# Performance work log

Measured on AMD Instinct MI355X. Metric: run time of the kernel, lower is better.

The kernel has to match this reference:

```python
import jax, jax.numpy as jnp
import numpy as np
import math

N, D, DV, B = 8192, 128, 128, 64
PHI_EPS = 1e-4
NORM_EPS = 1e-8


def _make_omega(dimv=128, dimqk=128, seed=0):
    # Faithful to FavorAttention._omega: QR of uniform blocks, rows renormalized
    # by norms of uniform rows, then transposed -> shape (dimqk, dimv).
    rng = np.random.default_rng(seed)
    nblocks = dimv // dimqk
    blocks = []
    for _ in range(nblocks):
        q, _ = np.linalg.qr(rng.random((dimqk, dimqk)))
        blocks.append(q.T)
    missing = dimv - nblocks * dimqk
    if missing > 0:
        q, _ = np.linalg.qr(rng.random((dimqk, dimqk)))
        blocks.append(q.T[:missing])
    norm = np.linalg.norm(rng.random((dimv, dimqk)), axis=1, keepdims=True)
    return (norm * np.vstack(blocks)).T.astype(np.float32)


def setup_inputs() -> dict:
    key = jax.random.key(0)
    kq, kk, kv, kb = jax.random.split(key, 4)
    Q = jax.random.normal(kq, (N, D), dtype=jnp.float32)
    K = jax.random.normal(kk, (N, D), dtype=jnp.float32)
    V = jax.random.normal(kv, (N, DV), dtype=jnp.float32)
    batch_seg = jnp.sort(jax.random.randint(kb, (N,), 0, B)).astype(jnp.int64)
    omega = jnp.asarray(_make_omega(128, 128))
    return {"Q": Q, "K": K, "V": V, "omega": omega,
            "batch_seg": batch_seg, "num_batch": B}


def _phi(x, omega, is_query, batch_seg, num_batch):
    d = x.shape[-1]
    m = omega.shape[-1]
    U = (x / d ** 0.25) @ omega                              # [n, m]
    h = jnp.sum(x * x, axis=-1, keepdims=True) / (2.0 * d ** 0.5)
    if is_query:
        maximum = jnp.max(U, axis=-1, keepdims=True)         # per-row max
    else:
        # per-segment max of masked U; original masks off-segment entries with 0,
        # so the effective per-segment max is clamped at 0.
        row_max = jnp.max(U, axis=-1)                        # [n]
        seg_max = jax.ops.segment_max(row_max, batch_seg, num_segments=num_batch)
        seg_max = jnp.maximum(seg_max, 0.0)
        maximum = seg_max[batch_seg][:, None]                # [n, 1]
    return (jnp.exp(U - h - maximum) + PHI_EPS) / math.sqrt(m)


def reference(Q, K, V, omega, batch_seg, num_batch):
    # FAVOR+ linear attention with segment-wise (per-molecule) normalization.
    Qp = _phi(Q, omega, True, batch_seg, num_batch)          # [n, m]
    Kp = _phi(K, omega, False, batch_seg, num_batch)         # [n, m]
    # norm_i = Qp_i . sum_{j in seg(i)} Kp_j  + eps
    Ksum = jax.ops.segment_sum(Kp, batch_seg, num_segments=num_batch)  # [B, m]
    norm = jnp.einsum('nm,nm->n', Qp, Ksum[batch_seg]) + NORM_EPS      # [n]
    # S_b = sum_{j in b} Kp_j (outer) V_j ; equals the masked (K Q^T)^T V of the
    # original, without materializing the n x n matrix.
    S = jax.ops.segment_sum(Kp[:, :, None] * V[:, None, :], batch_seg,
                            num_segments=num_batch)          # [B, m, dv]
    out = jnp.einsum('nm,nmd->nd', Qp, S[batch_seg]) / norm[:, None]
    return out
```

## Files before the change

### kernel.cpp

```cpp
#include <hip/hip_runtime.h>
#include <math.h>


#define NROWS 8192
#define DIM   128
#define NSEG  64

#define INV_D4      0.29730177875068026f
#define INV_SQRT_M  0.08838834764831845f
#define PHI_EPS_F   1e-4f
#define NORM_EPS_F  1e-8f

__global__ __launch_bounds__(256, 4) void k_phi(
    const float* __restrict__ Q, const float* __restrict__ K,
    const float* __restrict__ omega, const int* __restrict__ seg,
    float* __restrict__ Qp, float* __restrict__ UK,
    float* __restrict__ hK, int* __restrict__ segmax)
{
    __shared__ float xs[16][DIM];

    const int t = threadIdx.x;
    const int bid = blockIdx.x;
    const bool isQ = bid < 512;
    const int rowbase = (isQ ? bid : bid - 512) * 16;
    const float* X = (isQ ? Q : K) + (size_t)rowbase * DIM;

    {
        const float4* xg = (const float4*)X;
        float4* xd = (float4*)&xs[0][0];
#pragma unroll
        for (int s = 0; s < 2; ++s) {
            float4 v = xg[t + s * 256];
            v.x *= INV_D4; v.y *= INV_D4; v.z *= INV_D4; v.w *= INV_D4;
            xd[t + s * 256] = v;
        }
    }
    __syncthreads();

    const int w = t >> 6, lane = t & 63;
    const int rg = lane >> 5, cl = lane & 31;
    const int rA = w * 4 + rg * 2, rB = rA + 1;

    float hA, hB;
    {
        const float4 a = *(const float4*)&xs[rA][cl * 4];
        const float4 b = *(const float4*)&xs[rB][cl * 4];
        float pa = a.x * a.x + a.y * a.y + a.z * a.z + a.w * a.w;
        float pb = b.x * b.x + b.y * b.y + b.z * b.z + b.w * b.w;
#pragma unroll
        for (int m = 1; m < 32; m <<= 1) {
            pa += __shfl_xor(pa, m, 64);
            pb += __shfl_xor(pb, m, 64);
        }
        hA = 0.5f * pa; hB = 0.5f * pb;
    }

    float4 accA = make_float4(0.f, 0.f, 0.f, 0.f);
    float4 accB = make_float4(0.f, 0.f, 0.f, 0.f);

#pragma unroll 2
    for (int d = 0; d < DIM; d += 4) {
        const float4 o0 = *(const float4*)&omega[(size_t)(d + 0) * DIM + cl * 4];
        const float4 o1 = *(const float4*)&omega[(size_t)(d + 1) * DIM + cl * 4];
        const float4 o2 = *(const float4*)&omega[(size_t)(d + 2) * DIM + cl * 4];
        const float4 o3 = *(const float4*)&omega[(size_t)(d + 3) * DIM + cl * 4];
        const float4 xa = *(const float4*)&xs[rA][d];
        const float4 xb = *(const float4*)&xs[rB][d];
        accA.x = fmaf(xa.x, o0.x, fmaf(xa.y, o1.x, fmaf(xa.z, o2.x, fmaf(xa.w, o3.x, accA.x))));
        accA.y = fmaf(xa.x, o0.y, fmaf(xa.y, o1.y, fmaf(xa.z, o2.y, fmaf(xa.w, o3.y, accA.y))));
        accA.z = fmaf(xa.x, o0.z, fmaf(xa.y, o1.z, fmaf(xa.z, o2.z, fmaf(xa.w, o3.z, accA.z))));
        accA.w = fmaf(xa.x, o0.w, fmaf(xa.y, o1.w, fmaf(xa.z, o2.w, fmaf(xa.w, o3.w, accA.w))));
        accB.x = fmaf(xb.x, o0.x, fmaf(xb.y, o1.x, fmaf(xb.z, o2.x, fmaf(xb.w, o3.x, accB.x))));
        accB.y = fmaf(xb.x, o0.y, fmaf(xb.y, o1.y, fmaf(xb.z, o2.y, fmaf(xb.w, o3.y, accB.y))));
        accB.z = fmaf(xb.x, o0.z, fmaf(xb.y, o1.z, fmaf(xb.z, o2.z, fmaf(xb.w, o3.z, accB.z))));
        accB.w = fmaf(xb.x, o0.w, fmaf(xb.y, o1.w, fmaf(xb.z, o2.w, fmaf(xb.w, o3.w, accB.w))));
    }

    float mA = fmaxf(fmaxf(accA.x, accA.y), fmaxf(accA.z, accA.w));
    float mB = fmaxf(fmaxf(accB.x, accB.y), fmaxf(accB.z, accB.w));
#pragma unroll
    for (int m = 1; m < 32; m <<= 1) {
        mA = fmaxf(mA, __shfl_xor(mA, m, 64));
        mB = fmaxf(mB, __shfl_xor(mB, m, 64));
    }

    const int gA = rowbase + rA, gB = rowbase + rB;
    if (isQ) {
        const float bA = hA + mA, bB = hB + mB;
        float4 eA, eB;
        eA.x = (__expf(accA.x - bA) + PHI_EPS_F) * INV_SQRT_M;
        eA.y = (__expf(accA.y - bA) + PHI_EPS_F) * INV_SQRT_M;
        eA.z = (__expf(accA.z - bA) + PHI_EPS_F) * INV_SQRT_M;
        eA.w = (__expf(accA.w - bA) + PHI_EPS_F) * INV_SQRT_M;
        eB.x = (__expf(accB.x - bB) + PHI_EPS_F) * INV_SQRT_M;
        eB.y = (__expf(accB.y - bB) + PHI_EPS_F) * INV_SQRT_M;
        eB.z = (__expf(accB.z - bB) + PHI_EPS_F) * INV_SQRT_M;
        eB.w = (__expf(accB.w - bB) + PHI_EPS_F) * INV_SQRT_M;
        *(float4*)&Qp[(size_t)gA * DIM + cl * 4] = eA;
        *(float4*)&Qp[(size_t)gB * DIM + cl * 4] = eB;
    } else {
        *(float4*)&UK[(size_t)gA * DIM + cl * 4] = accA;
        *(float4*)&UK[(size_t)gB * DIM + cl * 4] = accB;
        if (cl == 0) {
            hK[gA] = hA; hK[gB] = hB;
            if (mA > 0.f) atomicMax(&segmax[seg[gA]], __float_as_int(mA));
            if (mB > 0.f) atomicMax(&segmax[seg[gB]], __float_as_int(mB));
        }
    }
}

__global__ __launch_bounds__(256, 4) void k_accum(
    const float* __restrict__ UK, const float* __restrict__ hK,
    const float* __restrict__ V, const int* __restrict__ seg,
    const float* __restrict__ segmaxf,
    float* __restrict__ S, float* __restrict__ Ksum)
{
    __shared__ float kp[32][32];
    __shared__ float vv[32][32];

    const int t = threadIdx.x;
    const int sid  = blockIdx.x >> 4;
    const int tile = blockIdx.x & 15;
    const int tm = (tile >> 2) * 32;
    const int tv = (tile & 3) * 32;

    int start, end;
    {
        int a = 0, b = NROWS;
        while (a < b) { int m = (a + b) >> 1; if (seg[m] < sid) a = m + 1; else b = m; }
        start = a; b = NROWS;
        while (a < b) { int m = (a + b) >> 1; if (seg[m] < sid + 1) a = m + 1; else b = m; }
        end = a;
    }

    const float smax = segmaxf[sid];
    const int rs = t >> 3;
    const int cs = (t & 7) * 4;
    const int ty = t >> 4;
    const int tx = t & 15;

    float a00 = 0.f, a01 = 0.f, a10 = 0.f, a11 = 0.f;
    float4 ksl = make_float4(0.f, 0.f, 0.f, 0.f);

    for (int j = start; j < end; j += 32) {
        const int row = j + rs;
        float4 kpv = make_float4(0.f, 0.f, 0.f, 0.f);
        float4 vvv = make_float4(0.f, 0.f, 0.f, 0.f);
        if (row < end) {
            const float4 u = *(const float4*)&UK[(size_t)row * DIM + tm + cs];
            const float h = hK[row] + smax;
            kpv.x = (__expf(u.x - h) + PHI_EPS_F) * INV_SQRT_M;
            kpv.y = (__expf(u.y - h) + PHI_EPS_F) * INV_SQRT_M;
            kpv.z = (__expf(u.z - h) + PHI_EPS_F) * INV_SQRT_M;
            kpv.w = (__expf(u.w - h) + PHI_EPS_F) * INV_SQRT_M;
            vvv = *(const float4*)&V[(size_t)row * DIM + tv + cs];
        }
        __syncthreads();
        *(float4*)&kp[rs][cs] = kpv;
        *(float4*)&vv[rs][cs] = vvv;
        ksl.x += kpv.x; ksl.y += kpv.y; ksl.z += kpv.z; ksl.w += kpv.w;
        __syncthreads();
#pragma unroll
        for (int k = 0; k < 32; ++k) {
            const float2 ka = *(const float2*)&kp[k][ty * 2];
            const float2 vb = *(const float2*)&vv[k][tx * 2];
            a00 = fmaf(ka.x, vb.x, a00);
            a01 = fmaf(ka.x, vb.y, a01);
            a10 = fmaf(ka.y, vb.x, a10);
            a11 = fmaf(ka.y, vb.y, a11);
        }
    }

    float* Sseg = S + (size_t)sid * DIM * DIM;
    {
        float2 r0; r0.x = a00; r0.y = a01;
        float2 r1; r1.x = a10; r1.y = a11;
        *(float2*)&Sseg[(tm + 2 * ty + 0) * DIM + tv + 2 * tx] = r0;
        *(float2*)&Sseg[(tm + 2 * ty + 1) * DIM + tv + 2 * tx] = r1;
    }

    __syncthreads();
    *(float4*)&kp[rs][cs] = ksl;
    __syncthreads();
    if (tv == 0 && t < 32) {
        float s = 0.f;
#pragma unroll
        for (int r = 0; r < 32; ++r) s += kp[r][t];
        Ksum[sid * DIM + tm + t] = s;
    }
}

__global__ __launch_bounds__(256, 4) void k_out(
    const float* __restrict__ Qp, const float* __restrict__ S,
    const float* __restrict__ Ksum, const int* __restrict__ seg,
    float* __restrict__ out)
{
    __shared__ float qs[16][DIM];

    const int t = threadIdx.x;
    const int rowbase = blockIdx.x * 16;

    {
        const float4* xg = (const float4*)(Qp + (size_t)rowbase * DIM);
        float4* xd = (float4*)&qs[0][0];
#pragma unroll
        for (int s = 0; s < 2; ++s) xd[t + s * 256] = xg[t + s * 256];
    }
    __syncthreads();

    const int w = t >> 6, lane = t & 63;
    const int rg = lane >> 5, cl = lane & 31;
    const int rA = w * 4 + rg * 2, rB = rA + 1;
    const int gA = rowbase + rA, gB = rowbase + rB;
    const int sA = seg[gA], sB = seg[gB];
    const float* SA = S + (size_t)sA * DIM * DIM;
    const float* SB = S + (size_t)sB * DIM * DIM;

    float nA, nB;
    {
        const float4 qa = *(const float4*)&qs[rA][cl * 4];
        const float4 qb = *(const float4*)&qs[rB][cl * 4];
        const float4 ka = *(const float4*)&Ksum[sA * DIM + cl * 4];
        const float4 kb = *(const float4*)&Ksum[sB * DIM + cl * 4];
        float pa = qa.x * ka.x + qa.y * ka.y + qa.z * ka.z + qa.w * ka.w;
        float pb = qb.x * kb.x + qb.y * kb.y + qb.z * kb.z + qb.w * kb.w;
#pragma unroll
        for (int m = 1; m < 32; m <<= 1) {
            pa += __shfl_xor(pa, m, 64);
            pb += __shfl_xor(pb, m, 64);
        }
        nA = pa + NORM_EPS_F; nB = pb + NORM_EPS_F;
    }

    float4 accA = make_float4(0.f, 0.f, 0.f, 0.f);
    float4 accB = make_float4(0.f, 0.f, 0.f, 0.f);

#pragma unroll 2
    for (int m = 0; m < DIM; m += 4) {
        const float4 qa = *(const float4*)&qs[rA][m];
        const float4 qb = *(const float4*)&qs[rB][m];
        const float4 a0 = *(const float4*)&SA[(size_t)(m + 0) * DIM + cl * 4];
        const float4 a1 = *(const float4*)&SA[(size_t)(m + 1) * DIM + cl * 4];
        const float4 a2 = *(const float4*)&SA[(size_t)(m + 2) * DIM + cl * 4];
        const float4 a3 = *(const float4*)&SA[(size_t)(m + 3) * DIM + cl * 4];
        const float4 b0 = *(const float4*)&SB[(size_t)(m + 0) * DIM + cl * 4];
        const float4 b1 = *(const float4*)&SB[(size_t)(m + 1) * DIM + cl * 4];
        const float4 b2 = *(const float4*)&SB[(size_t)(m + 2) * DIM + cl * 4];
        const float4 b3 = *(const float4*)&SB[(size_t)(m + 3) * DIM + cl * 4];
        accA.x = fmaf(qa.x, a0.x, fmaf(qa.y, a1.x, fmaf(qa.z, a2.x, fmaf(qa.w, a3.x, accA.x))));
        accA.y = fmaf(qa.x, a0.y, fmaf(qa.y, a1.y, fmaf(qa.z, a2.y, fmaf(qa.w, a3.y, accA.y))));
        accA.z = fmaf(qa.x, a0.z, fmaf(qa.y, a1.z, fmaf(qa.z, a2.z, fmaf(qa.w, a3.z, accA.z))));
        accA.w = fmaf(qa.x, a0.w, fmaf(qa.y, a1.w, fmaf(qa.z, a2.w, fmaf(qa.w, a3.w, accA.w))));
        accB.x = fmaf(qb.x, b0.x, fmaf(qb.y, b1.x, fmaf(qb.z, b2.x, fmaf(qb.w, b3.x, accB.x))));
        accB.y = fmaf(qb.x, b0.y, fmaf(qb.y, b1.y, fmaf(qb.z, b2.y, fmaf(qb.w, b3.y, accB.y))));
        accB.z = fmaf(qb.x, b0.z, fmaf(qb.y, b1.z, fmaf(qb.z, b2.z, fmaf(qb.w, b3.z, accB.z))));
        accB.w = fmaf(qb.x, b0.w, fmaf(qb.y, b1.w, fmaf(qb.z, b2.w, fmaf(qb.w, b3.w, accB.w))));
    }

    const float iA = 1.0f / nA, iB = 1.0f / nB;
    float4 oA, oB;
    oA.x = accA.x * iA; oA.y = accA.y * iA; oA.z = accA.z * iA; oA.w = accA.w * iA;
    oB.x = accB.x * iB; oB.y = accB.y * iB; oB.z = accB.z * iB; oB.w = accB.w * iB;
    *(float4*)&out[(size_t)gA * DIM + cl * 4] = oA;
    *(float4*)&out[(size_t)gB * DIM + cl * 4] = oB;
}

extern "C" void kernel_launch(void* const* d_in, const int* in_sizes, int n_in,
                              void* d_out, int out_size, void* d_ws, size_t ws_size,
                              hipStream_t stream)
{
    const float* Q     = (const float*)d_in[0];
    const float* K     = (const float*)d_in[1];
    const float* V     = (const float*)d_in[2];
    const float* omega = (const float*)d_in[3];
    const int*   seg   = (const int*)d_in[4];
    float* out = (float*)d_out;

    float* ws      = (float*)d_ws;
    float* S       = ws;
    float* Ksum    = S + (size_t)NSEG * DIM * DIM;
    float* segmaxf = Ksum + NSEG * DIM;
    float* Qp      = segmaxf + NSEG;
    float* UK      = Qp + (size_t)NROWS * DIM;
    float* hK      = UK + (size_t)NROWS * DIM;

    hipMemsetAsync(segmaxf, 0, NSEG * sizeof(float), stream);

    hipLaunchKernelGGL(k_phi, dim3(1024), dim3(256), 0, stream,
                       Q, K, omega, seg, Qp, UK, hK, (int*)segmaxf);
    hipLaunchKernelGGL(k_accum, dim3(NSEG * 16), dim3(256), 0, stream,
                       UK, hK, V, seg, segmaxf, S, Ksum);
    hipLaunchKernelGGL(k_out, dim3(512), dim3(256), 0, stream,
                       Qp, S, Ksum, seg, out);
}
```

Baseline: 164.1 us.

## Tile phi and output kernels 4 rows per thread, segment-grouped output blocks

k_phi now processes 32 rows per block with 4 rows per thread, and software-prefetches omega in a double-buffered register scheme so each omega load is reused across 4 rows. k_out is reorganized so each block handles one segment (binary-searching its row range) and iterates over that segment's rows in 32-row chunks, giving every row in a chunk the same S matrix. That reuse of S and Ksum cuts redundant global/L2 traffic. The cost is more registers (launch bounds lowered to 2), fewer blocks, and possible load imbalance when segment sizes vary.

```diff
diff --git a/kernel.cpp b/kernel.cpp
--- a/kernel.cpp
+++ b/kernel.cpp
@@ -11,25 +11,35 @@
 #define PHI_EPS_F   1e-4f
 #define NORM_EPS_F  1e-8f
 
-__global__ __launch_bounds__(256, 4) void k_phi(
+#define FMA4x4(acc, xa, o0, o1, o2, o3)                                   \
+    acc.x = fmaf(xa.x, o0.x, acc.x); acc.x = fmaf(xa.y, o1.x, acc.x);     \
+    acc.x = fmaf(xa.z, o2.x, acc.x); acc.x = fmaf(xa.w, o3.x, acc.x);     \
+    acc.y = fmaf(xa.x, o0.y, acc.y); acc.y = fmaf(xa.y, o1.y, acc.y);     \
+    acc.y = fmaf(xa.z, o2.y, acc.y); acc.y = fmaf(xa.w, o3.y, acc.y);     \
+    acc.z = fmaf(xa.x, o0.z, acc.z); acc.z = fmaf(xa.y, o1.z, acc.z);     \
+    acc.z = fmaf(xa.z, o2.z, acc.z); acc.z = fmaf(xa.w, o3.z, acc.z);     \
+    acc.w = fmaf(xa.x, o0.w, acc.w); acc.w = fmaf(xa.y, o1.w, acc.w);     \
+    acc.w = fmaf(xa.z, o2.w, acc.w); acc.w = fmaf(xa.w, o3.w, acc.w);
+
+__global__ __launch_bounds__(256, 2) void k_phi(
     const float* __restrict__ Q, const float* __restrict__ K,
     const float* __restrict__ omega, const int* __restrict__ seg,
     float* __restrict__ Qp, float* __restrict__ UK,
     float* __restrict__ hK, int* __restrict__ segmax)
 {
-    __shared__ float xs[16][DIM];
+    __shared__ float xs[32][DIM];
 
     const int t = threadIdx.x;
     const int bid = blockIdx.x;
-    const bool isQ = bid < 512;
-    const int rowbase = (isQ ? bid : bid - 512) * 16;
+    const bool isQ = bid < 256;
+    const int rowbase = (isQ ? bid : bid - 256) * 32;
     const float* X = (isQ ? Q : K) + (size_t)rowbase * DIM;
 
     {
         const float4* xg = (const float4*)X;
         float4* xd = (float4*)&xs[0][0];
 #pragma unroll
-        for (int s = 0; s < 2; ++s) {
+        for (int s = 0; s < 4; ++s) {
             float4 v = xg[t + s * 256];
             v.x *= INV_D4; v.y *= INV_D4; v.z *= INV_D4; v.w *= INV_D4;
             xd[t + s * 256] = v;
@@ -39,72 +49,92 @@
 
     const int w = t >> 6, lane = t & 63;
     const int rg = lane >> 5, cl = lane & 31;
-    const int rA = w * 4 + rg * 2, rB = rA + 1;
-
-    float hA, hB;
-    {
-        const float4 a = *(const float4*)&xs[rA][cl * 4];
-        const float4 b = *(const float4*)&xs[rB][cl * 4];
-        float pa = a.x * a.x + a.y * a.y + a.z * a.z + a.w * a.w;
-        float pb = b.x * b.x + b.y * b.y + b.z * b.z + b.w * b.w;
-#pragma unroll
-        for (int m = 1; m < 32; m <<= 1) {
-            pa += __shfl_xor(pa, m, 64);
-            pb += __shfl_xor(pb, m, 64);
-        }
-        hA = 0.5f * pa; hB = 0.5f * pb;
-    }
-
-    float4 accA = make_float4(0.f, 0.f, 0.f, 0.f);
-    float4 accB = make_float4(0.f, 0.f, 0.f, 0.f);
-
-#pragma unroll 2
-    for (int d = 0; d < DIM; d += 4) {
-        const float4 o0 = *(const float4*)&omega[(size_t)(d + 0) * DIM + cl * 4];
-        const float4 o1 = *(const float4*)&omega[(size_t)(d + 1) * DIM + cl * 4];
-        const float4 o2 = *(const float4*)&omega[(size_t)(d + 2) * DIM + cl * 4];
-        const float4 o3 = *(const float4*)&omega[(size_t)(d + 3) * DIM + cl * 4];
-        const float4 xa = *(const float4*)&xs[rA][d];
-        const float4 xb = *(const float4*)&xs[rB][d];
-        accA.x = fmaf(xa.x, o0.x, fmaf(xa.y, o1.x, fmaf(xa.z, o2.x, fmaf(xa.w, o3.x, accA.x))));
-        accA.y = fmaf(xa.x, o0.y, fmaf(xa.y, o1.y, fmaf(xa.z, o2.y, fmaf(xa.w, o3.y, accA.y))));
-        accA.z = fmaf(xa.x, o0.z, fmaf(xa.y, o1.z, fmaf(xa.z, o2.z, fmaf(xa.w, o3.z, accA.z))));
-        accA.w = fmaf(xa.x, o0.w, fmaf(xa.y, o1.w, fmaf(xa.z, o2.w, fmaf(xa.w, o3.w, accA.w))));
-        accB.x = fmaf(xb.x, o0.x, fmaf(xb.y, o1.x, fmaf(xb.z, o2.x, fmaf(xb.w, o3.x, accB.x))));
-        accB.y = fmaf(xb.x, o0.y, fmaf(xb.y, o1.y, fmaf(xb.z, o2.y, fmaf(xb.w, o3.y, accB.y))));
-        accB.z = fmaf(xb.x, o0.z, fmaf(xb.y, o1.z, fmaf(xb.z, o2.z, fmaf(xb.w, o3.z, accB.z))));
-        accB.w = fmaf(xb.x, o0.w, fmaf(xb.y, o1.w, fmaf(xb.z, o2.w, fmaf(xb.w, o3.w, accB.w))));
-    }
-
-    float mA = fmaxf(fmaxf(accA.x, accA.y), fmaxf(accA.z, accA.w));
-    float mB = fmaxf(fmaxf(accB.x, accB.y), fmaxf(accB.z, accB.w));
-#pragma unroll
-    for (int m = 1; m < 32; m <<= 1) {
-        mA = fmaxf(mA, __shfl_xor(mA, m, 64));
-        mB = fmaxf(mB, __shfl_xor(mB, m, 64));
-    }
-
-    const int gA = rowbase + rA, gB = rowbase + rB;
-    if (isQ) {
-        const float bA = hA + mA, bB = hB + mB;
-        float4 eA, eB;
-        eA.x = (__expf(accA.x - bA) + PHI_EPS_F) * INV_SQRT_M;
-        eA.y = (__expf(accA.y - bA) + PHI_EPS_F) * INV_SQRT_M;
-        eA.z = (__expf(accA.z - bA) + PHI_EPS_F) * INV_SQRT_M;
-        eA.w = (__expf(accA.w - bA) + PHI_EPS_F) * INV_SQRT_M;
-        eB.x = (__expf(accB.x - bB) + PHI_EPS_F) * INV_SQRT_M;
-        eB.y = (__expf(accB.y - bB) + PHI_EPS_F) * INV_SQRT_M;
-        eB.z = (__expf(accB.z - bB) + PHI_EPS_F) * INV_SQRT_M;
-        eB.w = (__expf(accB.w - bB) + PHI_EPS_F) * INV_SQRT_M;
-        *(float4*)&Qp[(size_t)gA * DIM + cl * 4] = eA;
-        *(float4*)&Qp[(size_t)gB * DIM + cl * 4] = eB;
-    } else {
-        *(float4*)&UK[(size_t)gA * DIM + cl * 4] = accA;
-        *(float4*)&UK[(size_t)gB * DIM + cl * 4] = accB;
-        if (cl == 0) {
-            hK[gA] = hA; hK[gB] = hB;
-            if (mA > 0.f) atomicMax(&segmax[seg[gA]], __float_as_int(mA));
-            if (mB > 0.f) atomicMax(&segmax[seg[gB]], __float_as_int(mB));
+    int r[4];
+#pragma unroll
+    for (int i = 0; i < 4; ++i) r[i] = w * 8 + 2 * i + rg;
+
+    float h[4];
+#pragma unroll
+    for (int i = 0; i < 4; ++i) {
+        const float4 a = *(const float4*)&xs[r[i]][cl * 4];
+        float p = a.x * a.x + a.y * a.y + a.z * a.z + a.w * a.w;
+#pragma unroll
+        for (int m = 1; m < 32; m <<= 1) p += __shfl_xor(p, m, 64);
+        h[i] = 0.5f * p;
+    }
+
+    float4 acc[4];
+#pragma unroll
+    for (int i = 0; i < 4; ++i) acc[i] = make_float4(0.f, 0.f, 0.f, 0.f);
+
+    const float4* og = (const float4*)omega;
+    float4 oa0, oa1, oa2, oa3, ob0, ob1, ob2, ob3;
+    oa0 = og[0 * 32 + cl]; oa1 = og[1 * 32 + cl];
+    oa2 = og[2 * 32 + cl]; oa3 = og[3 * 32 + cl];
+    ob0 = og[4 * 32 + cl]; ob1 = og[5 * 32 + cl];
+    ob2 = og[6 * 32 + cl]; ob3 = og[7 * 32 + cl];
+
+#pragma unroll 1
+    for (int d = 0; d < DIM; d += 8) {
+        {
+            float4 xa0 = *(const float4*)&xs[r[0]][d];
+            float4 xa1 = *(const float4*)&xs[r[1]][d];
+            float4 xa2 = *(const float4*)&xs[r[2]][d];
+            float4 xa3 = *(const float4*)&xs[r[3]][d];
+            FMA4x4(acc[0], xa0, oa0, oa1, oa2, oa3);
+            FMA4x4(acc[1], xa1, oa0, oa1, oa2, oa3);
+            FMA4x4(acc[2], xa2, oa0, oa1, oa2, oa3);
+            FMA4x4(acc[3], xa3, oa0, oa1, oa2, oa3);
+        }
+        {
+            const int dn = (d + 8) & 127;
+            oa0 = og[(dn + 0) * 32 + cl]; oa1 = og[(dn + 1) * 32 + cl];
+            oa2 = og[(dn + 2) * 32 + cl]; oa3 = og[(dn + 3) * 32 + cl];
+        }
+        {
+            float4 xb0 = *(const float4*)&xs[r[0]][d + 4];
+            float4 xb1 = *(const float4*)&xs[r[1]][d + 4];
+            float4 xb2 = *(const float4*)&xs[r[2]][d + 4];
+            float4 xb3 = *(const float4*)&xs[r[3]][d + 4];
+            FMA4x4(acc[0], xb0, ob0, ob1, ob2, ob3);
+            FMA4x4(acc[1], xb1, ob0, ob1, ob2, ob3);
+            FMA4x4(acc[2], xb2, ob0, ob1, ob2, ob3);
+            FMA4x4(acc[3], xb3, ob0, ob1, ob2, ob3);
+        }
+        {
+            const int dn = (d + 12) & 127;
+            ob0 = og[(dn + 0) * 32 + cl]; ob1 = og[(dn + 1) * 32 + cl];
+            ob2 = og[(dn + 2) * 32 + cl]; ob3 = og[(dn + 3) * 32 + cl];
+        }
+    }
+
+    float mx[4];
+#pragma unroll
+    for (int i = 0; i < 4; ++i) {
+        float m = fmaxf(fmaxf(acc[i].x, acc[i].y), fmaxf(acc[i].z, acc[i].w));
+#pragma unroll
+        for (int s = 1; s < 32; s <<= 1) m = fmaxf(m, __shfl_xor(m, s, 64));
+        mx[i] = m;
+    }
+
+#pragma unroll
+    for (int i = 0; i < 4; ++i) {
+        const int gr = rowbase + r[i];
+        if (isQ) {
+            const float b = h[i] + mx[i];
+            float4 o;
+            o.x = (__expf(acc[i].x - b) + PHI_EPS_F) * INV_SQRT_M;
+            o.y = (__expf(acc[i].y - b) + PHI_EPS_F) * INV_SQRT_M;
+            o.z = (__expf(acc[i].z - b) + PHI_EPS_F) * INV_SQRT_M;
+            o.w = (__expf(acc[i].w - b) + PHI_EPS_F) * INV_SQRT_M;
+            *(float4*)&Qp[(size_t)gr * DIM + cl * 4] = o;
+        } else {
+            *(float4*)&UK[(size_t)gr * DIM + cl * 4] = acc[i];
+            if (cl == 0) {
+                hK[gr] = h[i];
+                if (mx[i] > 0.f)
+                    atomicMax(&segmax[seg[gr]], __float_as_int(mx[i]));
+            }
         }
     }
 }
@@ -190,79 +220,113 @@
     }
 }
 
-__global__ __launch_bounds__(256, 4) void k_out(
+__global__ __launch_bounds__(256, 2) void k_out(
     const float* __restrict__ Qp, const float* __restrict__ S,
     const float* __restrict__ Ksum, const int* __restrict__ seg,
     float* __restrict__ out)
 {
-    __shared__ float qs[16][DIM];
+    __shared__ float qs[32][DIM];
 
     const int t = threadIdx.x;
-    const int rowbase = blockIdx.x * 16;
-
+    const int sid = blockIdx.x >> 3, part = blockIdx.x & 7;
+
+    int start, end;
     {
-        const float4* xg = (const float4*)(Qp + (size_t)rowbase * DIM);
-        float4* xd = (float4*)&qs[0][0];
-#pragma unroll
-        for (int s = 0; s < 2; ++s) xd[t + s * 256] = xg[t + s * 256];
-    }
-    __syncthreads();
+        int a = 0, b = NROWS;
+        while (a < b) { int m = (a + b) >> 1; if (seg[m] < sid) a = m + 1; else b = m; }
+        start = a; b = NROWS;
+        while (a < b) { int m = (a + b) >> 1; if (seg[m] < sid + 1) a = m + 1; else b = m; }
+        end = a;
+    }
 
     const int w = t >> 6, lane = t & 63;
     const int rg = lane >> 5, cl = lane & 31;
-    const int rA = w * 4 + rg * 2, rB = rA + 1;
-    const int gA = rowbase + rA, gB = rowbase + rB;
-    const int sA = seg[gA], sB = seg[gB];
-    const float* SA = S + (size_t)sA * DIM * DIM;
-    const float* SB = S + (size_t)sB * DIM * DIM;
-
-    float nA, nB;
-    {
-        const float4 qa = *(const float4*)&qs[rA][cl * 4];
-        const float4 qb = *(const float4*)&qs[rB][cl * 4];
-        const float4 ka = *(const float4*)&Ksum[sA * DIM + cl * 4];
-        const float4 kb = *(const float4*)&Ksum[sB * DIM + cl * 4];
-        float pa = qa.x * ka.x + qa.y * ka.y + qa.z * ka.z + qa.w * ka.w;
-        float pb = qb.x * kb.x + qb.y * kb.y + qb.z * kb.z + qb.w * kb.w;
-#pragma unroll
-        for (int m = 1; m < 32; m <<= 1) {
-            pa += __shfl_xor(pa, m, 64);
-            pb += __shfl_xor(pb, m, 64);
-        }
-        nA = pa + NORM_EPS_F; nB = pb + NORM_EPS_F;
-    }
-
-    float4 accA = make_float4(0.f, 0.f, 0.f, 0.f);
-    float4 accB = make_float4(0.f, 0.f, 0.f, 0.f);
-
-#pragma unroll 2
-    for (int m = 0; m < DIM; m += 4) {
-        const float4 qa = *(const float4*)&qs[rA][m];
-        const float4 qb = *(const float4*)&qs[rB][m];
-        const float4 a0 = *(const float4*)&SA[(size_t)(m + 0) * DIM + cl * 4];
-        const float4 a1 = *(const float4*)&SA[(size_t)(m + 1) * DIM + cl * 4];
-        const float4 a2 = *(const float4*)&SA[(size_t)(m + 2) * DIM + cl * 4];
-        const float4 a3 = *(const float4*)&SA[(size_t)(m + 3) * DIM + cl * 4];
-        const float4 b0 = *(const float4*)&SB[(size_t)(m + 0) * DIM + cl * 4];
-        const float4 b1 = *(const float4*)&SB[(size_t)(m + 1) * DIM + cl * 4];
-        const float4 b2 = *(const float4*)&SB[(size_t)(m + 2) * DIM + cl * 4];
-        const float4 b3 = *(const float4*)&SB[(size_t)(m + 3) * DIM + cl * 4];
-        accA.x = fmaf(qa.x, a0.x, fmaf(qa.y, a1.x, fmaf(qa.z, a2.x, fmaf(qa.w, a3.x, accA.x))));
-        accA.y = fmaf(qa.x, a0.y, fmaf(qa.y, a1.y, fmaf(qa.z, a2.y, fmaf(qa.w, a3.y, accA.y))));
-        accA.z = fmaf(qa.x, a0.z, fmaf(qa.y, a1.z, fmaf(qa.z, a2.z, fmaf(qa.w, a3.z, accA.z))));
-        accA.w = fmaf(qa.x, a0.w, fmaf(qa.y, a1.w, fmaf(qa.z, a2.w, fmaf(qa.w, a3.w, accA.w))));
-        accB.x = fmaf(qb.x, b0.x, fmaf(qb.y, b1.x, fmaf(qb.z, b2.x, fmaf(qb.w, b3.x, accB.x))));
-        accB.y = fmaf(qb.x, b0.y, fmaf(qb.y, b1.y, fmaf(qb.z, b2.y, fmaf(qb.w, b3.y, accB.y))));
-        accB.z = fmaf(qb.x, b0.z, fmaf(qb.y, b1.z, fmaf(qb.z, b2.z, fmaf(qb.w, b3.z, accB.z))));
-        accB.w = fmaf(qb.x, b0.w, fmaf(qb.y, b1.w, fmaf(qb.z, b2.w, fmaf(qb.w, b3.w, accB.w))));
-    }
-
-    const float iA = 1.0f / nA, iB = 1.0f / nB;
-    float4 oA, oB;
-    oA.x = accA.x * iA; oA.y = accA.y * iA; oA.z = accA.z * iA; oA.w = accA.w * iA;
-    oB.x = accB.x * iB; oB.y = accB.y * iB; oB.z = accB.z * iB; oB.w = accB.w * iB;
-    *(float4*)&out[(size_t)gA * DIM + cl * 4] = oA;
-    *(float4*)&out[(size_t)gB * DIM + cl * 4] = oB;
+    int r[4];
+#pragma unroll
+    for (int i = 0; i < 4; ++i) r[i] = w * 8 + 2 * i + rg;
+
+    const float4 ks = *(const float4*)&Ksum[sid * DIM + cl * 4];
+    const float4* sg = (const float4*)(S + (size_t)sid * DIM * DIM);
+
+    for (int base = start + part * 32; base < end; base += 256) {
+        __syncthreads();
+        {
+            float4* xd = (float4*)&qs[0][0];
+#pragma unroll
+            for (int s = 0; s < 4; ++s) {
+                const int idx = t + s * 256;
+                const int grow = min(base + (idx >> 5), end - 1);
+                xd[idx] = ((const float4*)(Qp + (size_t)grow * DIM))[idx & 31];
+            }
+        }
+        __syncthreads();
+
+        float n[4];
+#pragma unroll
+        for (int i = 0; i < 4; ++i) {
+            const float4 q = *(const float4*)&qs[r[i]][cl * 4];
+            float p = q.x * ks.x + q.y * ks.y + q.z * ks.z + q.w * ks.w;
+#pragma unroll
+            for (int m = 1; m < 32; m <<= 1) p += __shfl_xor(p, m, 64);
+            n[i] = p + NORM_EPS_F;
+        }
+
+        float4 acc[4];
+#pragma unroll
+        for (int i = 0; i < 4; ++i) acc[i] = make_float4(0.f, 0.f, 0.f, 0.f);
+
+        float4 sa0, sa1, sa2, sa3, sb0, sb1, sb2, sb3;
+        sa0 = sg[0 * 32 + cl]; sa1 = sg[1 * 32 + cl];
+        sa2 = sg[2 * 32 + cl]; sa3 = sg[3 * 32 + cl];
+        sb0 = sg[4 * 32 + cl]; sb1 = sg[5 * 32 + cl];
+        sb2 = sg[6 * 32 + cl]; sb3 = sg[7 * 32 + cl];
+
+#pragma unroll 1
+        for (int m = 0; m < DIM; m += 8) {
+            {
+                float4 xa0 = *(const float4*)&qs[r[0]][m];
+                float4 xa1 = *(const float4*)&qs[r[1]][m];
+                float4 xa2 = *(const float4*)&qs[r[2]][m];
+                float4 xa3 = *(const float4*)&qs[r[3]][m];
+                FMA4x4(acc[0], xa0, sa0, sa1, sa2, sa3);
+                FMA4x4(acc[1], xa1, sa0, sa1, sa2, sa3);
+                FMA4x4(acc[2], xa2, sa0, sa1, sa2, sa3);
+                FMA4x4(acc[3], xa3, sa0, sa1, sa2, sa3);
+            }
+            {
+                const int mn = (m + 8) & 127;
+                sa0 = sg[(mn + 0) * 32 + cl]; sa1 = sg[(mn + 1) * 32 + cl];
+                sa2 = sg[(mn + 2) * 32 + cl]; sa3 = sg[(mn + 3) * 32 + cl];
+            }
+            {
+                float4 xb0 = *(const float4*)&qs[r[0]][m + 4];
+                float4 xb1 = *(const float4*)&qs[r[1]][m + 4];
+                float4 xb2 = *(const float4*)&qs[r[2]][m + 4];
+                float4 xb3 = *(const float4*)&qs[r[3]][m + 4];
+                FMA4x4(acc[0], xb0, sb0, sb1, sb2, sb3);
+                FMA4x4(acc[1], xb1, sb0, sb1, sb2, sb3);
+                FMA4x4(acc[2], xb2, sb0, sb1, sb2, sb3);
+                FMA4x4(acc[3], xb3, sb0, sb1, sb2, sb3);
+            }
+            {
+                const int mn = (m + 12) & 127;
+                sb0 = sg[(mn + 0) * 32 + cl]; sb1 = sg[(mn + 1) * 32 + cl];
+                sb2 = sg[(mn + 2) * 32 + cl]; sb3 = sg[(mn + 3) * 32 + cl];
+            }
+        }
+
+#pragma unroll
+        for (int i = 0; i < 4; ++i) {
+            const int gr = base + r[i];
+            if (gr < end) {
+                const float inv = 1.0f / n[i];
+                float4 o;
+                o.x = acc[i].x * inv; o.y = acc[i].y * inv;
+                o.z = acc[i].z * inv; o.w = acc[i].w * inv;
+                *(float4*)&out[(size_t)gr * DIM + cl * 4] = o;
+            }
+        }
+    }
 }
 
 extern "C" void kernel_launch(void* const* d_in, const int* in_sizes, int n_in,
@@ -286,10 +350,10 @@
 
     hipMemsetAsync(segmaxf, 0, NSEG * sizeof(float), stream);
 
-    hipLaunchKernelGGL(k_phi, dim3(1024), dim3(256), 0, stream,
+    hipLaunchKernelGGL(k_phi, dim3(512), dim3(256), 0, stream,
                        Q, K, omega, seg, Qp, UK, hK, (int*)segmaxf);
     hipLaunchKernelGGL(k_accum, dim3(NSEG * 16), dim3(256), 0, stream,
                        UK, hK, V, seg, segmaxf, S, Ksum);
-    hipLaunchKernelGGL(k_out, dim3(512), dim3(256), 0, stream,
+    hipLaunchKernelGGL(k_out, dim3(NSEG * 8), dim3(256), 0, stream,
                        Qp, S, Ksum, seg, out);
 }
```

Measured after the change: 205.0 us. 24.9% more time.
